# Performance work log

Hardware: AMD Instinct MI355X
Metric: run time of the kernel (lower is better)

The kernel has to match this reference:

```python
import jax, jax.numpy as jnp
import numpy as np

N, C, F, E = 32768, 256, 1024, 16
TOP_K = 2


def setup_inputs() -> dict:
    key = jax.random.key(0)
    k_x, k_gw, k_w1, k_w2 = jax.random.split(key, 4)
    x = jax.random.normal(k_x, (N, C), dtype=jnp.float32)
    gate_W = jax.random.normal(k_gw, (E, C), dtype=jnp.float32) * 0.01  # nn.init.normal_(std=0.01)
    gate_b = jnp.zeros((E,), dtype=jnp.float32)
    W1 = jax.random.normal(k_w1, (E, C, F), dtype=jnp.float32) * 0.02
    b1 = jnp.zeros((E, F), dtype=jnp.float32)
    W2 = jax.random.normal(k_w2, (E, F, C), dtype=jnp.float32) * 0.02
    b2 = jnp.zeros((E, C), dtype=jnp.float32)
    return {"x": x, "gate_W": gate_W, "gate_b": gate_b,
            "W1": W1, "b1": b1, "W2": W2, "b2": b2}


def reference(x, gate_W, gate_b, W1, b1, W2, b2):
    # Gating (eval mode: no gaussian noise)
    gate_logits = x @ gate_W.T + gate_b                       # [N, E]
    gate_probs = jax.nn.softmax(gate_logits, axis=-1)
    gate_entropy = -(gate_probs * jnp.log(gate_probs + 1e-8)).sum(axis=-1).mean()

    topk_val, topk_idx = jax.lax.top_k(gate_logits, TOP_K)   # [N, K]
    gate_weights = jax.nn.softmax(topk_val, axis=-1)          # softmax over the top-k logits

    # Dense all-expert FFN compute (matches the torch stack over experts)
    h = jax.nn.relu(jnp.einsum('nc,ecf->enf', x, W1) + b1[:, None, :])   # [E, N, F]
    expert_outputs = jnp.einsum('enf,efc->enc', h, W2) + b2[:, None, :]  # [E, N, C]

    # Gather top-k expert outputs per token and combine
    eo = jnp.transpose(expert_outputs, (1, 0, 2))             # [N, E, C]
    selected = jnp.take_along_axis(eo, topk_idx[:, :, None], axis=1)  # [N, K, C]
    out = (gate_weights[:, :, None] * selected).sum(axis=1)  # [N, C]

    # default args: return_gate=False, return_entropy=True
    return out, gate_entropy
```

## Files before the change

### kernel.cpp

```cpp
#include <hip/hip_runtime.h>
#include <hip/hip_bf16.h>
#include <math.h>

#define N_TOK 32768
#define C_DIM 256
#define F_DIM 1024
#define E_NUM 16
#define TILE_R 128
#define NCH 32
#define NBLK 544

typedef unsigned short u16;
typedef unsigned int u32;
typedef __attribute__((ext_vector_type(4))) u16 u16x4;
typedef __attribute__((ext_vector_type(8))) u16 u16x8;
typedef __attribute__((ext_vector_type(8))) short bf16x8;
typedef __attribute__((ext_vector_type(4))) u32 u32x4;
typedef __attribute__((ext_vector_type(16))) float f32x16;

#define AS1 __attribute__((address_space(1)))
#define AS3 __attribute__((address_space(3)))

__device__ __forceinline__ void gload16(const void* g, void* lds) {
    __builtin_amdgcn_global_load_lds((const AS1 u32*)(uintptr_t)g,
                                     (AS3 u32*)(u32)(uintptr_t)lds, 16, 0, 0);
}

__device__ __forceinline__ u16 f2bf(float f) {
    union { float f; u32 u; } v; v.f = f;
    u32 r = v.u + 0x7fffu + ((v.u >> 16) & 1u);
    return (u16)(r >> 16);
}

__device__ __forceinline__ float bf2f(u16 b) {
    union { u32 u; float f; } v; v.u = ((u32)b) << 16;
    return v.f;
}


__global__ __launch_bounds__(256) void gate_kernel(
    const float* __restrict__ x, const float* __restrict__ gW,
    const float* __restrict__ gb, float* __restrict__ ent_out,
    int* __restrict__ tidx, float* __restrict__ tw, int* __restrict__ counts,
    u16* __restrict__ xb)
{
    __shared__ float gws[E_NUM * C_DIM];
    __shared__ float gbs[E_NUM];
    __shared__ float went[4];
    __shared__ int lc[E_NUM];
    int tid = threadIdx.x;

    for (int i = tid; i < E_NUM * C_DIM / 4; i += 256)
        ((float4*)gws)[i] = ((const float4*)gW)[i];
    if (tid < E_NUM) { gbs[tid] = gb[tid]; lc[tid] = 0; }
    __syncthreads();

    int tok = tid >> 2, q = tid & 3;
    int n = blockIdx.x * 64 + tok;
    const float* xr = x + (size_t)n * C_DIM;

    float4 xv[16];
    #pragma unroll
    for (int j = 0; j < 16; j++)
        xv[j] = *(const float4*)(xr + j * 16 + q * 4);

    #pragma unroll
    for (int j = 0; j < 16; j++) {
        u16x4 o;
        o[0] = f2bf(xv[j].x); o[1] = f2bf(xv[j].y);
        o[2] = f2bf(xv[j].z); o[3] = f2bf(xv[j].w);
        *(u16x4*)(xb + (size_t)n * C_DIM + j * 16 + q * 4) = o;
    }

    float lg[E_NUM];
    #pragma unroll
    for (int e = 0; e < E_NUM; e++) lg[e] = 0.f;
    #pragma unroll
    for (int j = 0; j < 16; j++) {
        #pragma unroll
        for (int e = 0; e < E_NUM; e++) {
            float4 g = *(const float4*)(gws + e * C_DIM + j * 16 + q * 4);
            lg[e] += xv[j].x * g.x + xv[j].y * g.y + xv[j].z * g.z + xv[j].w * g.w;
        }
    }
    #pragma unroll
    for (int e = 0; e < E_NUM; e++) {
        lg[e] += __shfl_xor(lg[e], 1);
        lg[e] += __shfl_xor(lg[e], 2);
        lg[e] += gbs[e];
    }

    float m = lg[0];
    #pragma unroll
    for (int e = 1; e < E_NUM; e++) m = fmaxf(m, lg[e]);
    float s = 0.f, ex[E_NUM];
    #pragma unroll
    for (int e = 0; e < E_NUM; e++) { ex[e] = __expf(lg[e] - m); s += ex[e]; }
    float inv = 1.f / s;
    float ent = 0.f;
    #pragma unroll
    for (int e = 0; e < E_NUM; e++) {
        float p = ex[e] * inv;
        ent -= p * logf(p + 1e-8f);
    }

    float v0 = -1e30f, v1 = -1e30f;
    int i0 = 0, i1 = 0;
    #pragma unroll
    for (int e = 0; e < E_NUM; e++) {
        float l = lg[e];
        if (l > v0) { v1 = v0; i1 = i0; v0 = l; i0 = e; }
        else if (l > v1) { v1 = l; i1 = e; }
    }
    if (q == 0) {
        float w1e = __expf(v1 - v0);
        float z = 1.f + w1e;
        tidx[2 * n] = i0; tidx[2 * n + 1] = i1;
        tw[2 * n] = 1.f / z; tw[2 * n + 1] = w1e / z;
        atomicAdd(&lc[i0], 1);
        atomicAdd(&lc[i1], 1);
    }

    float v = ent;
    for (int off = 32; off > 0; off >>= 1) v += __shfl_down(v, off);
    int wid = tid >> 6, lane = tid & 63;
    if (lane == 0) went[wid] = v;
    __syncthreads();
    if (tid == 0)
        atomicAdd(ent_out, (went[0] + went[1] + went[2] + went[3]) * (1.0f / (4.0f * N_TOK)));
    if (tid < E_NUM && lc[tid]) atomicAdd(&counts[tid], lc[tid]);
}

__global__ void prefix_kernel(const int* __restrict__ counts,
                              int* __restrict__ offs, int* __restrict__ tp)
{
    if (threadIdx.x == 0 && blockIdx.x == 0) {
        int o = 0, t = 0;
        offs[0] = 0; tp[0] = 0;
        for (int e = 0; e < E_NUM; e++) {
            o += counts[e];
            t += (counts[e] + TILE_R - 1) / TILE_R;
            offs[e + 1] = o;
            tp[e + 1] = t;
        }
    }
}

__global__ __launch_bounds__(256) void scatter_kernel(
    const int* __restrict__ tidx, const float* __restrict__ tw,
    const int* __restrict__ offs, int* __restrict__ fill,
    int* __restrict__ tok, float* __restrict__ wgt, int* __restrict__ pairpos)
{
    __shared__ int lc[E_NUM], lbase[E_NUM];
    int tid = threadIdx.x;
    if (tid < E_NUM) lc[tid] = 0;
    __syncthreads();
    int n = blockIdx.x * 256 + tid;
    int e0 = tidx[2 * n], e1 = tidx[2 * n + 1];
    int r0 = atomicAdd(&lc[e0], 1);
    int r1 = atomicAdd(&lc[e1], 1);
    __syncthreads();
    if (tid < E_NUM) lbase[tid] = offs[tid] + atomicAdd(&fill[tid], lc[tid]);
    __syncthreads();
    int p0 = lbase[e0] + r0, p1 = lbase[e1] + r1;
    tok[p0] = n; wgt[p0] = tw[2 * n];     pairpos[2 * n] = p0;
    tok[p1] = n; wgt[p1] = tw[2 * n + 1]; pairpos[2 * n + 1] = p1;
}

__global__ __launch_bounds__(256) void tcvt_w1f(
    const float* __restrict__ W1, u16* __restrict__ w1f)
{
    __shared__ float t[256][33];
    int e = blockIdx.x, ft = blockIdx.y;
    int tid = threadIdx.x;
    const float* src = W1 + ((size_t)e * C_DIM) * F_DIM + (size_t)tid * F_DIM + ft * 32;
    #pragma unroll
    for (int j = 0; j < 8; j++) {
        float4 v = *(const float4*)(src + j * 4);
        t[tid][j * 4] = v.x; t[tid][j * 4 + 1] = v.y;
        t[tid][j * 4 + 2] = v.z; t[tid][j * 4 + 3] = v.w;
    }
    __syncthreads();
    int l = tid & 63, ksq = tid >> 6;
    #pragma unroll
    for (int p = 0; p < 4; p++) {
        int ks = ksq * 4 + p;
        int c0 = ks * 16 + (l >> 5) * 8;
        u16x8 o;
        #pragma unroll
        for (int j = 0; j < 8; j++) o[j] = f2bf(t[c0 + j][l & 31]);
        *(u16x8*)(w1f + ((size_t)((e * 32 + ft) * 16 + ks)) * 512 + l * 8) = o;
    }
}

__global__ __launch_bounds__(256) void tcvt_w2f(
    const float* __restrict__ W2, u16* __restrict__ w2f)
{
    __shared__ float t[256][33];
    int e = blockIdx.x, ct = blockIdx.y, fq = blockIdx.z;
    int tid = threadIdx.x;
    const float* src = W2 + ((size_t)e * F_DIM + fq * 256 + tid) * C_DIM + ct * 32;
    #pragma unroll
    for (int j = 0; j < 8; j++) {
        float4 v = *(const float4*)(src + j * 4);
        t[tid][j * 4] = v.x; t[tid][j * 4 + 1] = v.y;
        t[tid][j * 4 + 2] = v.z; t[tid][j * 4 + 3] = v.w;
    }
    __syncthreads();
    int l = tid & 63, kq = tid >> 6;
    #pragma unroll
    for (int p = 0; p < 4; p++) {
        int kfl = kq * 4 + p;
        int f0 = kfl * 16 + (l >> 5) * 8;
        u16x8 o;
        #pragma unroll
        for (int j = 0; j < 8; j++) o[j] = f2bf(t[f0 + j][l & 31]);
        *(u16x8*)(w2f + ((size_t)((e * 8 + ct) * 64 + fq * 16 + kfl)) * 512 + l * 8) = o;
    }
}

#define B1S_OFF 65536

#define STAGE_CHUNK(CHN, NBUF)                                                \
    {                                                                         \
        _Pragma("unroll")                                                     \
        for (int i = 0; i < 4; i++) {                                         \
            int ks = (wid << 2) + i;                                          \
            gload16(w1fe + (((size_t)((CHN) << 4) + ks) << 9) + (lane << 3),  \
                    (NBUF) + (ks << 10));                                     \
        }                                                                     \
        _Pragma("unroll")                                                     \
        for (int i = 0; i < 4; i++) {                                         \
            int g = (wid << 2) + i;                                           \
            int ct = g >> 1, s2 = g & 1;                                      \
            gload16(w2fe + (((size_t)(ct << 6) + ((CHN) << 1) + s2) << 9) + (lane << 3), \
                    (NBUF) + 16384 + (g << 10));                              \
        }                                                                     \
    }

template <int MODE>
__global__ __launch_bounds__(256, 2) void ffn_mfma(
    const u16* __restrict__ xb, const u16* __restrict__ w1f,
    const u16* __restrict__ w2f, const float* __restrict__ b1,
    const float* __restrict__ b2, const int* __restrict__ tok,
    const float* __restrict__ wgt, const int* __restrict__ offs,
    const int* __restrict__ tp, u16* __restrict__ ybuf,
    float* __restrict__ out)
{
    __shared__ __align__(1024) char smem[70656];
    int* s_tok = (int*)(smem + 69632);
    float* s_w = (float*)(smem + 70144);
    float* b1s = (float*)(smem + B1S_OFF);

    int bidx = blockIdx.x;
    int b = (bidx & 7) * (NBLK / 8) + (bidx >> 3);
    if (b >= tp[E_NUM]) return;
    int e = 0;
    while (b >= tp[e + 1]) e++;
    int base = offs[e] + ((b - tp[e]) << 7);
    int rows = offs[e + 1] - base; if (rows > TILE_R) rows = TILE_R;

    int tid = threadIdx.x;
    int lane = tid & 63, wid = tid >> 6;
    int hi = lane >> 5;

    const u16* w1fe = w1f + ((size_t)e << 9) * 512;
    const u16* w2fe = w2f + ((size_t)e << 9) * 512;
    const float* b1e = b1 + e * F_DIM;
    const float* b2e = b2 + e * C_DIM;

    if (tid < TILE_R) {
        int src = (tid < rows) ? base + tid : base;
        s_tok[tid] = tok[src];
        s_w[tid] = (tid < rows) ? wgt[src] : 0.f;
    }
    ((float4*)b1s)[tid] = ((const float4*)b1e)[tid];
    __syncthreads();

    #pragma unroll
    for (int i = 0; i < 16; i++) {
        int idx2 = (wid << 4) + i;
        int row = ((idx2 >> 4) << 5) + (lane & 31);
        gload16(xb + ((size_t)s_tok[row] << 8) + ((idx2 & 15) << 4) + (hi << 3),
                smem + (idx2 << 10));
    }
    asm volatile("s_waitcnt vmcnt(0)" ::: "memory");
    __syncthreads();

    bf16x8 xr[16];
    #pragma unroll
    for (int ks = 0; ks < 16; ks++)
        xr[ks] = *(const bf16x8*)(smem + (wid << 14) + (ks << 10) + (lane << 4));
    __syncthreads();

    STAGE_CHUNK(0, smem)
    asm volatile("s_waitcnt vmcnt(0)" ::: "memory");
    __syncthreads();

    f32x16 acc2[8];
    #pragma unroll
    for (int ct = 0; ct < 8; ct++) acc2[ct] = (f32x16)(0.0f);

    for (int ch = 0; ch < NCH; ch++) {
        int cur = ch & 1;
        const char* cbuf = smem + (cur << 15);

        if (ch + 1 < NCH) {
            char* nbuf = smem + ((cur ^ 1) << 15);
            STAGE_CHUNK(ch + 1, nbuf)
        }

        const char* w1b = cbuf + (lane << 4);
        f32x16 acc1a = (f32x16)(0.0f), acc1b = (f32x16)(0.0f);
        #pragma unroll
        for (int ks = 0; ks < 8; ks++) {
            bf16x8 a0 = *(const bf16x8*)(w1b + ((2 * ks) << 10));
            bf16x8 a1 = *(const bf16x8*)(w1b + ((2 * ks + 1) << 10));
            acc1a = __builtin_amdgcn_mfma_f32_32x32x16_bf16(a0, xr[2 * ks], acc1a, 0, 0, 0);
            acc1b = __builtin_amdgcn_mfma_f32_32x32x16_bf16(a1, xr[2 * ks + 1], acc1b, 0, 0, 0);
        }

        float h[16];
        #pragma unroll
        for (int r = 0; r < 16; r++) {
            int fl = (r & 3) + ((r >> 2) << 3) + (hi << 2);
            h[r] = fmaxf(acc1a[r] + acc1b[r] + b1s[(ch << 5) + fl], 0.f);
        }
        u32 w[8];
        #pragma unroll
        for (int t = 0; t < 8; t++)
            asm("v_cvt_pk_bf16_f32 %0, %1, %2" : "=v"(w[t]) : "v"(h[2 * t]), "v"(h[2 * t + 1]));
        asm volatile("v_permlane32_swap_b32 %0, %1" : "+v"(w[0]), "+v"(w[2]));
        asm volatile("v_permlane32_swap_b32 %0, %1" : "+v"(w[1]), "+v"(w[3]));
        asm volatile("v_permlane32_swap_b32 %0, %1" : "+v"(w[4]), "+v"(w[6]));
        asm volatile("v_permlane32_swap_b32 %0, %1" : "+v"(w[5]), "+v"(w[7]));
        union { u32x4 u; bf16x8 v; } fr0, fr1;
        fr0.u = (u32x4){w[0], w[1], w[2], w[3]};
        fr1.u = (u32x4){w[4], w[5], w[6], w[7]};

        const char* w2b = cbuf + 16384 + (lane << 4);
        #pragma unroll
        for (int ctl = 0; ctl < 8; ctl++) {
            bf16x8 a0 = *(const bf16x8*)(w2b + ((ctl << 1) << 10));
            bf16x8 a1 = *(const bf16x8*)(w2b + (((ctl << 1) + 1) << 10));
            acc2[ctl] = __builtin_amdgcn_mfma_f32_32x32x16_bf16(a0, fr0.v, acc2[ctl], 0, 0, 0);
            acc2[ctl] = __builtin_amdgcn_mfma_f32_32x32x16_bf16(a1, fr1.v, acc2[ctl], 0, 0, 0);
        }

        asm volatile("s_waitcnt vmcnt(0) lgkmcnt(0)" ::: "memory");
        __builtin_amdgcn_s_barrier();
        __builtin_amdgcn_sched_barrier(0);
    }

    int m = (wid << 5) + (lane & 31);
    if (m < rows) {
        if (MODE == 0) {
            u16* yr = ybuf + ((size_t)(base + m) << 8);
            #pragma unroll
            for (int ctl = 0; ctl < 8; ctl++) {
                #pragma unroll
                for (int rq = 0; rq < 4; rq++) {
                    int c = (ctl << 5) + (rq << 3) + (hi << 2);
                    u16x4 o;
                    o[0] = f2bf(acc2[ctl][4 * rq]);
                    o[1] = f2bf(acc2[ctl][4 * rq + 1]);
                    o[2] = f2bf(acc2[ctl][4 * rq + 2]);
                    o[3] = f2bf(acc2[ctl][4 * rq + 3]);
                    *(u16x4*)(yr + c) = o;
                }
            }
        } else {
            float wgt_m = s_w[m];
            float* orow = out + ((size_t)s_tok[m] << 8);
            #pragma unroll
            for (int ctl = 0; ctl < 8; ctl++) {
                #pragma unroll
                for (int rq = 0; rq < 4; rq++) {
                    int c = (ctl << 5) + (rq << 3) + (hi << 2);
                    #pragma unroll
                    for (int l2 = 0; l2 < 4; l2++)
                        atomicAdd(&orow[c + l2],
                                  wgt_m * (acc2[ctl][4 * rq + l2] + b2e[c + l2]));
                }
            }
        }
    }
}

__global__ __launch_bounds__(256) void combine_kernel(
    const u16* __restrict__ ybuf, const int* __restrict__ tidx,
    const float* __restrict__ tw, const int* __restrict__ pairpos,
    const float* __restrict__ b2, float* __restrict__ out)
{
    int idx = blockIdx.x * 256 + threadIdx.x;
    int n = idx >> 6;
    int q = (idx & 63) << 2;
    int e0 = tidx[2 * n], e1 = tidx[2 * n + 1];
    float w0 = tw[2 * n], w1 = tw[2 * n + 1];
    int p0 = pairpos[2 * n], p1 = pairpos[2 * n + 1];
    u16x4 y0 = *(const u16x4*)(ybuf + ((size_t)p0 << 8) + q);
    u16x4 y1 = *(const u16x4*)(ybuf + ((size_t)p1 << 8) + q);
    float4 c0 = *(const float4*)(b2 + (e0 << 8) + q);
    float4 c1 = *(const float4*)(b2 + (e1 << 8) + q);
    float4 o;
    o.x = w0 * (bf2f(y0[0]) + c0.x) + w1 * (bf2f(y1[0]) + c1.x);
    o.y = w0 * (bf2f(y0[1]) + c0.y) + w1 * (bf2f(y1[1]) + c1.y);
    o.z = w0 * (bf2f(y0[2]) + c0.z) + w1 * (bf2f(y1[2]) + c1.z);
    o.w = w0 * (bf2f(y0[3]) + c0.w) + w1 * (bf2f(y1[3]) + c1.w);
    *(float4*)(out + ((size_t)n << 8) + q) = o;
}

extern "C" void kernel_launch(void* const* d_in, const int* in_sizes, int n_in,
                              void* d_out, int out_size, void* d_ws, size_t ws_size,
                              hipStream_t stream)
{
    const float* x   = (const float*)d_in[0];
    const float* gW  = (const float*)d_in[1];
    const float* gb  = (const float*)d_in[2];
    const float* W1  = (const float*)d_in[3];
    const float* b1  = (const float*)d_in[4];
    const float* W2  = (const float*)d_in[5];
    const float* b2  = (const float*)d_in[6];
    float* out = (float*)d_out;

    char* ws = (char*)d_ws;
    int*   topk_idx = (int*)(ws + 0);
    float* topk_w   = (float*)(ws + 262144);
    int*   tok      = (int*)(ws + 524288);
    float* wgt      = (float*)(ws + 786432);
    int*   pairpos  = (int*)(ws + 1048576);
    int*   counts   = (int*)(ws + 1310720);
    int*   fill     = (int*)(ws + 1310784);
    int*   offs     = (int*)(ws + 1310848);
    int*   tp       = (int*)(ws + 1310916);

    const size_t XB_OFF  = 2097152;
    const size_t W1F_OFF = 18874368;
    const size_t W2F_OFF = 27262976;
    const size_t Y_OFF   = 35651584;
    const size_t WS_FULL = Y_OFF + (size_t)2 * N_TOK * C_DIM * 2;

    u16* xb  = (u16*)(ws + XB_OFF);
    u16* w1f = (u16*)(ws + W1F_OFF);
    u16* w2f = (u16*)(ws + W2F_OFF);
    u16* ybuf = (u16*)(ws + Y_OFF);

    int mode = (ws_size >= WS_FULL) ? 0 : 1;

    float* ent_out = out + (size_t)N_TOK * C_DIM;

    if (mode == 0) {
        hipMemsetAsync(ent_out, 0, sizeof(float), stream);
    } else {
        hipMemsetAsync(d_out, 0, (size_t)(N_TOK * C_DIM + 1) * sizeof(float), stream);
    }
    hipMemsetAsync(counts, 0, 2 * E_NUM * sizeof(int), stream);

    gate_kernel<<<N_TOK / 64, 256, 0, stream>>>(x, gW, gb, ent_out,
                                                topk_idx, topk_w, counts, xb);
    prefix_kernel<<<1, 64, 0, stream>>>(counts, offs, tp);
    scatter_kernel<<<N_TOK / 256, 256, 0, stream>>>(topk_idx, topk_w, offs,
                                                    fill, tok, wgt, pairpos);
    tcvt_w1f<<<dim3(E_NUM, 32), 256, 0, stream>>>(W1, w1f);
    tcvt_w2f<<<dim3(E_NUM, 8, 4), 256, 0, stream>>>(W2, w2f);

    if (mode == 0) {
        ffn_mfma<0><<<NBLK, 256, 0, stream>>>(xb, w1f, w2f, b1, b2, tok, wgt,
                                              offs, tp, ybuf, out);
        combine_kernel<<<N_TOK * 64 / 256, 256, 0, stream>>>(ybuf, topk_idx,
                                                             topk_w, pairpos, b2, out);
    } else {
        ffn_mfma<1><<<NBLK, 256, 0, stream>>>(xb, w1f, w2f, b1, b2, tok, wgt,
                                              offs, tp, ybuf, out);
    }
}
```

Baseline: 181.7 us.

## Double rows per block so each wave computes two 32-row tiles sharing weight loads

Raises the token tile from 128 to 256 rows per block. Each wave now holds two sets of x fragments and accumulators, so every W1/W2 chunk staged into LDS feeds twice as many MFMAs. This halves weight traffic per token and the number of blocks. In exchange, register pressure roughly doubles, forcing one block per CU instead of two. There are also fewer, larger blocks, which risks tail imbalance and more padding waste on each expert's last tile.

```diff
diff --git a/kernel.cpp b/kernel.cpp
--- a/kernel.cpp
+++ b/kernel.cpp
@@ -6,9 +6,9 @@
 #define C_DIM 256
 #define F_DIM 1024
 #define E_NUM 16
-#define TILE_R 128
+#define TILE_R 256
 #define NCH 32
-#define NBLK 544
+#define NBLK 272
 
 typedef unsigned short u16;
 typedef unsigned int u32;
@@ -238,8 +238,62 @@
         }                                                                     \
     }
 
+#define REPACK(AA, AB, FR0, FR1)                                              \
+    {                                                                         \
+        float h[16];                                                          \
+        _Pragma("unroll")                                                     \
+        for (int r = 0; r < 16; r++) {                                        \
+            int fl = (r & 3) + ((r >> 2) << 3) + (hi << 2);                   \
+            h[r] = fmaxf((AA)[r] + (AB)[r] + b1s[(ch << 5) + fl], 0.f);       \
+        }                                                                     \
+        u32 w[8];                                                             \
+        _Pragma("unroll")                                                     \
+        for (int t = 0; t < 8; t++)                                           \
+            asm("v_cvt_pk_bf16_f32 %0, %1, %2" : "=v"(w[t]) : "v"(h[2 * t]), "v"(h[2 * t + 1])); \
+        asm volatile("v_permlane32_swap_b32 %0, %1" : "+v"(w[0]), "+v"(w[2]));\
+        asm volatile("v_permlane32_swap_b32 %0, %1" : "+v"(w[1]), "+v"(w[3]));\
+        asm volatile("v_permlane32_swap_b32 %0, %1" : "+v"(w[4]), "+v"(w[6]));\
+        asm volatile("v_permlane32_swap_b32 %0, %1" : "+v"(w[5]), "+v"(w[7]));\
+        (FR0).u = (u32x4){w[0], w[1], w[2], w[3]};                            \
+        (FR1).u = (u32x4){w[4], w[5], w[6], w[7]};                            \
+    }
+
+#define EPILOGUE_TILE(ACC, MIDX)                                              \
+    if ((MIDX) < rows) {                                                      \
+        if (MODE == 0) {                                                      \
+            u16* yr = ybuf + ((size_t)(base + (MIDX)) << 8);                  \
+            _Pragma("unroll")                                                 \
+            for (int ctl = 0; ctl < 8; ctl++) {                               \
+                _Pragma("unroll")                                             \
+                for (int rq = 0; rq < 4; rq++) {                              \
+                    int c = (ctl << 5) + (rq << 3) + (hi << 2);               \
+                    u16x4 o;                                                  \
+                    o[0] = f2bf((ACC)[ctl][4 * rq]);                          \
+                    o[1] = f2bf((ACC)[ctl][4 * rq + 1]);                      \
+                    o[2] = f2bf((ACC)[ctl][4 * rq + 2]);                      \
+                    o[3] = f2bf((ACC)[ctl][4 * rq + 3]);                      \
+                    *(u16x4*)(yr + c) = o;                                    \
+                }                                                             \
+            }                                                                 \
+        } else {                                                              \
+            float wgt_m = s_w[(MIDX)];                                        \
+            float* orow = out + ((size_t)s_tok[(MIDX)] << 8);                 \
+            _Pragma("unroll")                                                 \
+            for (int ctl = 0; ctl < 8; ctl++) {                               \
+                _Pragma("unroll")                                             \
+                for (int rq = 0; rq < 4; rq++) {                              \
+                    int c = (ctl << 5) + (rq << 3) + (hi << 2);               \
+                    _Pragma("unroll")                                         \
+                    for (int l2 = 0; l2 < 4; l2++)                            \
+                        atomicAdd(&orow[c + l2],                              \
+                                  wgt_m * ((ACC)[ctl][4 * rq + l2] + b2e[c + l2])); \
+                }                                                             \
+            }                                                                 \
+        }                                                                     \
+    }
+
 template <int MODE>
-__global__ __launch_bounds__(256, 2) void ffn_mfma(
+__global__ __launch_bounds__(256, 1) void ffn_mfma(
     const u16* __restrict__ xb, const u16* __restrict__ w1f,
     const u16* __restrict__ w2f, const float* __restrict__ b1,
     const float* __restrict__ b2, const int* __restrict__ tok,
@@ -247,9 +301,9 @@
     const int* __restrict__ tp, u16* __restrict__ ybuf,
     float* __restrict__ out)
 {
-    __shared__ __align__(1024) char smem[70656];
+    __shared__ __align__(1024) char smem[71680];
     int* s_tok = (int*)(smem + 69632);
-    float* s_w = (float*)(smem + 70144);
+    float* s_w = (float*)(smem + 70656);
     float* b1s = (float*)(smem + B1S_OFF);
 
     int bidx = blockIdx.x;
@@ -257,7 +311,7 @@
     if (b >= tp[E_NUM]) return;
     int e = 0;
     while (b >= tp[e + 1]) e++;
-    int base = offs[e] + ((b - tp[e]) << 7);
+    int base = offs[e] + ((b - tp[e]) << 8);
     int rows = offs[e + 1] - base; if (rows > TILE_R) rows = TILE_R;
 
     int tid = threadIdx.x;
@@ -277,29 +331,40 @@
     ((float4*)b1s)[tid] = ((const float4*)b1e)[tid];
     __syncthreads();
 
-    #pragma unroll
-    for (int i = 0; i < 16; i++) {
-        int idx2 = (wid << 4) + i;
-        int row = ((idx2 >> 4) << 5) + (lane & 31);
-        gload16(xb + ((size_t)s_tok[row] << 8) + ((idx2 & 15) << 4) + (hi << 3),
-                smem + (idx2 << 10));
-    }
-    asm volatile("s_waitcnt vmcnt(0)" ::: "memory");
-    __syncthreads();
-
-    bf16x8 xr[16];
-    #pragma unroll
-    for (int ks = 0; ks < 16; ks++)
-        xr[ks] = *(const bf16x8*)(smem + (wid << 14) + (ks << 10) + (lane << 4));
-    __syncthreads();
+    bf16x8 xrA[16], xrB[16];
+    #pragma unroll
+    for (int half = 0; half < 2; half++) {
+        #pragma unroll
+        for (int i = 0; i < 16; i++) {
+            int idx2 = (wid << 4) + i;
+            int row = ((idx2 >> 4) << 5) + (lane & 31) + (half << 7);
+            gload16(xb + ((size_t)s_tok[row] << 8) + ((idx2 & 15) << 4) + (hi << 3),
+                    smem + (idx2 << 10));
+        }
+        asm volatile("s_waitcnt vmcnt(0)" ::: "memory");
+        __syncthreads();
+        if (half == 0) {
+            #pragma unroll
+            for (int ks = 0; ks < 16; ks++)
+                xrA[ks] = *(const bf16x8*)(smem + (wid << 14) + (ks << 10) + (lane << 4));
+        } else {
+            #pragma unroll
+            for (int ks = 0; ks < 16; ks++)
+                xrB[ks] = *(const bf16x8*)(smem + (wid << 14) + (ks << 10) + (lane << 4));
+        }
+        __syncthreads();
+    }
 
     STAGE_CHUNK(0, smem)
     asm volatile("s_waitcnt vmcnt(0)" ::: "memory");
     __syncthreads();
 
-    f32x16 acc2[8];
-    #pragma unroll
-    for (int ct = 0; ct < 8; ct++) acc2[ct] = (f32x16)(0.0f);
+    f32x16 acc2A[8], acc2B[8];
+    #pragma unroll
+    for (int ct = 0; ct < 8; ct++) {
+        acc2A[ct] = (f32x16)(0.0f);
+        acc2B[ct] = (f32x16)(0.0f);
+    }
 
     for (int ch = 0; ch < NCH; ch++) {
         int cur = ch & 1;
@@ -311,40 +376,31 @@
         }
 
         const char* w1b = cbuf + (lane << 4);
-        f32x16 acc1a = (f32x16)(0.0f), acc1b = (f32x16)(0.0f);
+        f32x16 aAa = (f32x16)(0.0f), aAb = (f32x16)(0.0f);
+        f32x16 aBa = (f32x16)(0.0f), aBb = (f32x16)(0.0f);
         #pragma unroll
         for (int ks = 0; ks < 8; ks++) {
             bf16x8 a0 = *(const bf16x8*)(w1b + ((2 * ks) << 10));
             bf16x8 a1 = *(const bf16x8*)(w1b + ((2 * ks + 1) << 10));
-            acc1a = __builtin_amdgcn_mfma_f32_32x32x16_bf16(a0, xr[2 * ks], acc1a, 0, 0, 0);
-            acc1b = __builtin_amdgcn_mfma_f32_32x32x16_bf16(a1, xr[2 * ks + 1], acc1b, 0, 0, 0);
-        }
-
-        float h[16];
-        #pragma unroll
-        for (int r = 0; r < 16; r++) {
-            int fl = (r & 3) + ((r >> 2) << 3) + (hi << 2);
-            h[r] = fmaxf(acc1a[r] + acc1b[r] + b1s[(ch << 5) + fl], 0.f);
-        }
-        u32 w[8];
-        #pragma unroll
-        for (int t = 0; t < 8; t++)
-            asm("v_cvt_pk_bf16_f32 %0, %1, %2" : "=v"(w[t]) : "v"(h[2 * t]), "v"(h[2 * t + 1]));
-        asm volatile("v_permlane32_swap_b32 %0, %1" : "+v"(w[0]), "+v"(w[2]));
-        asm volatile("v_permlane32_swap_b32 %0, %1" : "+v"(w[1]), "+v"(w[3]));
-        asm volatile("v_permlane32_swap_b32 %0, %1" : "+v"(w[4]), "+v"(w[6]));
-        asm volatile("v_permlane32_swap_b32 %0, %1" : "+v"(w[5]), "+v"(w[7]));
-        union { u32x4 u; bf16x8 v; } fr0, fr1;
-        fr0.u = (u32x4){w[0], w[1], w[2], w[3]};
-        fr1.u = (u32x4){w[4], w[5], w[6], w[7]};
+            aAa = __builtin_amdgcn_mfma_f32_32x32x16_bf16(a0, xrA[2 * ks], aAa, 0, 0, 0);
+            aBa = __builtin_amdgcn_mfma_f32_32x32x16_bf16(a0, xrB[2 * ks], aBa, 0, 0, 0);
+            aAb = __builtin_amdgcn_mfma_f32_32x32x16_bf16(a1, xrA[2 * ks + 1], aAb, 0, 0, 0);
+            aBb = __builtin_amdgcn_mfma_f32_32x32x16_bf16(a1, xrB[2 * ks + 1], aBb, 0, 0, 0);
+        }
+
+        union { u32x4 u; bf16x8 v; } frA0, frA1, frB0, frB1;
+        REPACK(aAa, aAb, frA0, frA1)
+        REPACK(aBa, aBb, frB0, frB1)
 
         const char* w2b = cbuf + 16384 + (lane << 4);
         #pragma unroll
         for (int ctl = 0; ctl < 8; ctl++) {
             bf16x8 a0 = *(const bf16x8*)(w2b + ((ctl << 1) << 10));
             bf16x8 a1 = *(const bf16x8*)(w2b + (((ctl << 1) + 1) << 10));
-            acc2[ctl] = __builtin_amdgcn_mfma_f32_32x32x16_bf16(a0, fr0.v, acc2[ctl], 0, 0, 0);
-            acc2[ctl] = __builtin_amdgcn_mfma_f32_32x32x16_bf16(a1, fr1.v, acc2[ctl], 0, 0, 0);
+            acc2A[ctl] = __builtin_amdgcn_mfma_f32_32x32x16_bf16(a0, frA0.v, acc2A[ctl], 0, 0, 0);
+            acc2A[ctl] = __builtin_amdgcn_mfma_f32_32x32x16_bf16(a1, frA1.v, acc2A[ctl], 0, 0, 0);
+            acc2B[ctl] = __builtin_amdgcn_mfma_f32_32x32x16_bf16(a0, frB0.v, acc2B[ctl], 0, 0, 0);
+            acc2B[ctl] = __builtin_amdgcn_mfma_f32_32x32x16_bf16(a1, frB1.v, acc2B[ctl], 0, 0, 0);
         }
 
         asm volatile("s_waitcnt vmcnt(0) lgkmcnt(0)" ::: "memory");
@@ -352,39 +408,10 @@
         __builtin_amdgcn_sched_barrier(0);
     }
 
-    int m = (wid << 5) + (lane & 31);
-    if (m < rows) {
-        if (MODE == 0) {
-            u16* yr = ybuf + ((size_t)(base + m) << 8);
-            #pragma unroll
-            for (int ctl = 0; ctl < 8; ctl++) {
-                #pragma unroll
-                for (int rq = 0; rq < 4; rq++) {
-                    int c = (ctl << 5) + (rq << 3) + (hi << 2);
-                    u16x4 o;
-                    o[0] = f2bf(acc2[ctl][4 * rq]);
-                    o[1] = f2bf(acc2[ctl][4 * rq + 1]);
-                    o[2] = f2bf(acc2[ctl][4 * rq + 2]);
-                    o[3] = f2bf(acc2[ctl][4 * rq + 3]);
-                    *(u16x4*)(yr + c) = o;
-                }
-            }
-        } else {
-            float wgt_m = s_w[m];
-            float* orow = out + ((size_t)s_tok[m] << 8);
-            #pragma unroll
-            for (int ctl = 0; ctl < 8; ctl++) {
-                #pragma unroll
-                for (int rq = 0; rq < 4; rq++) {
-                    int c = (ctl << 5) + (rq << 3) + (hi << 2);
-                    #pragma unroll
-                    for (int l2 = 0; l2 < 4; l2++)
-                        atomicAdd(&orow[c + l2],
-                                  wgt_m * (acc2[ctl][4 * rq + l2] + b2e[c + l2]));
-                }
-            }
-        }
-    }
+    int mA = (wid << 5) + (lane & 31);
+    int mB = mA + 128;
+    EPILOGUE_TILE(acc2A, mA)
+    EPILOGUE_TILE(acc2B, mB)
 }
 
 __global__ __launch_bounds__(256) void combine_kernel(
```

Result: slower. 329.2 us (+81.2%).

## Load expert weight fragments directly from global memory into registers, drop LDS staging

Applied to the files above, without the earlier changes.

Removes the double-buffered LDS staging of W1/W2 chunks and the per-chunk barrier. Each wave now reads its weight fragments straight from global memory (through the cache) into registers just before the MFMAs. This saves LDS traffic and workgroup synchronisation. In exchange, every wave re-reads the same weights, the loads are no longer prefetched a chunk ahead, and register pressure rises from the 16-entry fragment arrays.

```diff
diff --git a/kernel.cpp b/kernel.cpp
--- a/kernel.cpp
+++ b/kernel.cpp
@@ -221,23 +221,6 @@
 
 #define B1S_OFF 65536
 
-#define STAGE_CHUNK(CHN, NBUF)                                                \
-    {                                                                         \
-        _Pragma("unroll")                                                     \
-        for (int i = 0; i < 4; i++) {                                         \
-            int ks = (wid << 2) + i;                                          \
-            gload16(w1fe + (((size_t)((CHN) << 4) + ks) << 9) + (lane << 3),  \
-                    (NBUF) + (ks << 10));                                     \
-        }                                                                     \
-        _Pragma("unroll")                                                     \
-        for (int i = 0; i < 4; i++) {                                         \
-            int g = (wid << 2) + i;                                           \
-            int ct = g >> 1, s2 = g & 1;                                      \
-            gload16(w2fe + (((size_t)(ct << 6) + ((CHN) << 1) + s2) << 9) + (lane << 3), \
-                    (NBUF) + 16384 + (g << 10));                              \
-        }                                                                     \
-    }
-
 template <int MODE>
 __global__ __launch_bounds__(256, 2) void ffn_mfma(
     const u16* __restrict__ xb, const u16* __restrict__ w1f,
@@ -291,33 +274,25 @@
     #pragma unroll
     for (int ks = 0; ks < 16; ks++)
         xr[ks] = *(const bf16x8*)(smem + (wid << 14) + (ks << 10) + (lane << 4));
-    __syncthreads();
-
-    STAGE_CHUNK(0, smem)
-    asm volatile("s_waitcnt vmcnt(0)" ::: "memory");
-    __syncthreads();
 
     f32x16 acc2[8];
     #pragma unroll
     for (int ct = 0; ct < 8; ct++) acc2[ct] = (f32x16)(0.0f);
 
+    const u16* w1p = w1fe + (lane << 3);
+    const u16* w2p = w2fe + (lane << 3);
+
     for (int ch = 0; ch < NCH; ch++) {
-        int cur = ch & 1;
-        const char* cbuf = smem + (cur << 15);
-
-        if (ch + 1 < NCH) {
-            char* nbuf = smem + ((cur ^ 1) << 15);
-            STAGE_CHUNK(ch + 1, nbuf)
-        }
-
-        const char* w1b = cbuf + (lane << 4);
+        bf16x8 wf[16];
+        #pragma unroll
+        for (int k = 0; k < 16; k++)
+            wf[k] = *(const bf16x8*)(w1p + (((size_t)(ch << 4) + k) << 9));
+
         f32x16 acc1a = (f32x16)(0.0f), acc1b = (f32x16)(0.0f);
         #pragma unroll
         for (int ks = 0; ks < 8; ks++) {
-            bf16x8 a0 = *(const bf16x8*)(w1b + ((2 * ks) << 10));
-            bf16x8 a1 = *(const bf16x8*)(w1b + ((2 * ks + 1) << 10));
-            acc1a = __builtin_amdgcn_mfma_f32_32x32x16_bf16(a0, xr[2 * ks], acc1a, 0, 0, 0);
-            acc1b = __builtin_amdgcn_mfma_f32_32x32x16_bf16(a1, xr[2 * ks + 1], acc1b, 0, 0, 0);
+            acc1a = __builtin_amdgcn_mfma_f32_32x32x16_bf16(wf[2 * ks], xr[2 * ks], acc1a, 0, 0, 0);
+            acc1b = __builtin_amdgcn_mfma_f32_32x32x16_bf16(wf[2 * ks + 1], xr[2 * ks + 1], acc1b, 0, 0, 0);
         }
 
         float h[16];
@@ -338,18 +313,17 @@
         fr0.u = (u32x4){w[0], w[1], w[2], w[3]};
         fr1.u = (u32x4){w[4], w[5], w[6], w[7]};
 
-        const char* w2b = cbuf + 16384 + (lane << 4);
+        bf16x8 wg[16];
+        #pragma unroll
+        for (int g = 0; g < 16; g++) {
+            int ct = g >> 1, s2 = g & 1;
+            wg[g] = *(const bf16x8*)(w2p + (((size_t)(ct << 6) + (ch << 1) + s2) << 9));
+        }
         #pragma unroll
         for (int ctl = 0; ctl < 8; ctl++) {
-            bf16x8 a0 = *(const bf16x8*)(w2b + ((ctl << 1) << 10));
-            bf16x8 a1 = *(const bf16x8*)(w2b + (((ctl << 1) + 1) << 10));
-            acc2[ctl] = __builtin_amdgcn_mfma_f32_32x32x16_bf16(a0, fr0.v, acc2[ctl], 0, 0, 0);
-            acc2[ctl] = __builtin_amdgcn_mfma_f32_32x32x16_bf16(a1, fr1.v, acc2[ctl], 0, 0, 0);
-        }
-
-        asm volatile("s_waitcnt vmcnt(0) lgkmcnt(0)" ::: "memory");
-        __builtin_amdgcn_s_barrier();
-        __builtin_amdgcn_sched_barrier(0);
+            acc2[ctl] = __builtin_amdgcn_mfma_f32_32x32x16_bf16(wg[2 * ctl], fr0.v, acc2[ctl], 0, 0, 0);
+            acc2[ctl] = __builtin_amdgcn_mfma_f32_32x32x16_bf16(wg[2 * ctl + 1], fr1.v, acc2[ctl], 0, 0, 0);
+        }
     }
 
     int m = (wid << 5) + (lane & 31);
```

Result: slower. 257.2 us (+41.6%).

## Halve FFN tile to 64 rows with 2-wave blocks and single-buffered weights

Applied to the files above, without the earlier changes.

Cuts the FFN tile from 128 to 64 tokens per block, uses 128-thread blocks, and raises the grid from 544 to 1040 blocks so more blocks can be resident. It drops the double-buffered weight staging for a single buffer loaded at the top of each chunk, with wave 0 loading W1 and wave 1 loading W2. This shrinks LDS to allow more blocks per CU. In exchange, each weight chunk is reused across half as many tokens, which doubles weight traffic, and load latency is no longer overlapped with MFMA work inside a block. Other parts of the kernel not shown, such as the x staging loop indexed by wid and the MODE 1 output path, may still assume the old 4-wave layout.

```diff
diff --git a/kernel.cpp b/kernel.cpp
--- a/kernel.cpp
+++ b/kernel.cpp
@@ -6,9 +6,9 @@
 #define C_DIM 256
 #define F_DIM 1024
 #define E_NUM 16
-#define TILE_R 128
+#define TILE_R 64
 #define NCH 32
-#define NBLK 544
+#define NBLK 1040
 
 typedef unsigned short u16;
 typedef unsigned int u32;
@@ -219,27 +219,25 @@
     }
 }
 
-#define B1S_OFF 65536
-
-#define STAGE_CHUNK(CHN, NBUF)                                                \
-    {                                                                         \
+#define B1S_OFF 32768
+
+#define STAGE_CHUNK(CHN)                                                      \
+    if (wid == 0) {                                                           \
         _Pragma("unroll")                                                     \
-        for (int i = 0; i < 4; i++) {                                         \
-            int ks = (wid << 2) + i;                                          \
-            gload16(w1fe + (((size_t)((CHN) << 4) + ks) << 9) + (lane << 3),  \
-                    (NBUF) + (ks << 10));                                     \
-        }                                                                     \
+        for (int k = 0; k < 16; k++)                                          \
+            gload16(w1fe + (((size_t)((CHN) << 4) + k) << 9) + (lane << 3),   \
+                    smem + (k << 10));                                        \
+    } else {                                                                  \
         _Pragma("unroll")                                                     \
-        for (int i = 0; i < 4; i++) {                                         \
-            int g = (wid << 2) + i;                                           \
+        for (int g = 0; g < 16; g++) {                                        \
             int ct = g >> 1, s2 = g & 1;                                      \
             gload16(w2fe + (((size_t)(ct << 6) + ((CHN) << 1) + s2) << 9) + (lane << 3), \
-                    (NBUF) + 16384 + (g << 10));                              \
+                    smem + 16384 + (g << 10));                                \
         }                                                                     \
     }
 
 template <int MODE>
-__global__ __launch_bounds__(256, 2) void ffn_mfma(
+__global__ __launch_bounds__(128, 4) void ffn_mfma(
     const u16* __restrict__ xb, const u16* __restrict__ w1f,
     const u16* __restrict__ w2f, const float* __restrict__ b1,
     const float* __restrict__ b2, const int* __restrict__ tok,
@@ -247,9 +245,9 @@
     const int* __restrict__ tp, u16* __restrict__ ybuf,
     float* __restrict__ out)
 {
-    __shared__ __align__(1024) char smem[70656];
-    int* s_tok = (int*)(smem + 69632);
-    float* s_w = (float*)(smem + 70144);
+    __shared__ __align__(1024) char smem[38400];
+    int* s_tok = (int*)(smem + 36864);
+    float* s_w = (float*)(smem + 37120);
     float* b1s = (float*)(smem + B1S_OFF);
 
     int bidx = blockIdx.x;
@@ -257,7 +255,7 @@
     if (b >= tp[E_NUM]) return;
     int e = 0;
     while (b >= tp[e + 1]) e++;
-    int base = offs[e] + ((b - tp[e]) << 7);
+    int base = offs[e] + ((b - tp[e]) << 6);
     int rows = offs[e + 1] - base; if (rows > TILE_R) rows = TILE_R;
 
     int tid = threadIdx.x;
@@ -274,7 +272,9 @@
         s_tok[tid] = tok[src];
         s_w[tid] = (tid < rows) ? wgt[src] : 0.f;
     }
-    ((float4*)b1s)[tid] = ((const float4*)b1e)[tid];
+    #pragma unroll
+    for (int i = 0; i < 2; i++)
+        ((float4*)b1s)[tid + i * 128] = ((const float4*)b1e)[tid + i * 128];
     __syncthreads();
 
     #pragma unroll
@@ -293,24 +293,17 @@
         xr[ks] = *(const bf16x8*)(smem + (wid << 14) + (ks << 10) + (lane << 4));
     __syncthreads();
 
-    STAGE_CHUNK(0, smem)
-    asm volatile("s_waitcnt vmcnt(0)" ::: "memory");
-    __syncthreads();
-
     f32x16 acc2[8];
     #pragma unroll
     for (int ct = 0; ct < 8; ct++) acc2[ct] = (f32x16)(0.0f);
 
     for (int ch = 0; ch < NCH; ch++) {
-        int cur = ch & 1;
-        const char* cbuf = smem + (cur << 15);
-
-        if (ch + 1 < NCH) {
-            char* nbuf = smem + ((cur ^ 1) << 15);
-            STAGE_CHUNK(ch + 1, nbuf)
-        }
-
-        const char* w1b = cbuf + (lane << 4);
+        STAGE_CHUNK(ch)
+        asm volatile("s_waitcnt vmcnt(0)" ::: "memory");
+        __builtin_amdgcn_s_barrier();
+        __builtin_amdgcn_sched_barrier(0);
+
+        const char* w1b = smem + (lane << 4);
         f32x16 acc1a = (f32x16)(0.0f), acc1b = (f32x16)(0.0f);
         #pragma unroll
         for (int ks = 0; ks < 8; ks++) {
@@ -338,16 +331,16 @@
         fr0.u = (u32x4){w[0], w[1], w[2], w[3]};
         fr1.u = (u32x4){w[4], w[5], w[6], w[7]};
 
-        const char* w2b = cbuf + 16384 + (lane << 4);
+        const char* w2b = smem + 16384 + (lane << 4);
         #pragma unroll
         for (int ctl = 0; ctl < 8; ctl++) {
-            bf16x8 a0 = *(const bf16x8*)(w2b + ((ctl << 1) << 10));
-            bf16x8 a1 = *(const bf16x8*)(w2b + (((ctl << 1) + 1) << 10));
-            acc2[ctl] = __builtin_amdgcn_mfma_f32_32x32x16_bf16(a0, fr0.v, acc2[ctl], 0, 0, 0);
-            acc2[ctl] = __builtin_amdgcn_mfma_f32_32x32x16_bf16(a1, fr1.v, acc2[ctl], 0, 0, 0);
-        }
-
-        asm volatile("s_waitcnt vmcnt(0) lgkmcnt(0)" ::: "memory");
+            bf16x8 b0 = *(const bf16x8*)(w2b + ((ctl << 1) << 10));
+            bf16x8 b1v = *(const bf16x8*)(w2b + (((ctl << 1) + 1) << 10));
+            acc2[ctl] = __builtin_amdgcn_mfma_f32_32x32x16_bf16(b0, fr0.v, acc2[ctl], 0, 0, 0);
+            acc2[ctl] = __builtin_amdgcn_mfma_f32_32x32x16_bf16(b1v, fr1.v, acc2[ctl], 0, 0, 0);
+        }
+
+        asm volatile("s_waitcnt lgkmcnt(0)" ::: "memory");
         __builtin_amdgcn_s_barrier();
         __builtin_amdgcn_sched_barrier(0);
     }
@@ -465,12 +458,12 @@
     tcvt_w2f<<<dim3(E_NUM, 8, 4), 256, 0, stream>>>(W2, w2f);
 
     if (mode == 0) {
-        ffn_mfma<0><<<NBLK, 256, 0, stream>>>(xb, w1f, w2f, b1, b2, tok, wgt,
+        ffn_mfma<0><<<NBLK, 128, 0, stream>>>(xb, w1f, w2f, b1, b2, tok, wgt,
                                               offs, tp, ybuf, out);
         combine_kernel<<<N_TOK * 64 / 256, 256, 0, stream>>>(ybuf, topk_idx,
                                                              topk_w, pairpos, b2, out);
     } else {
-        ffn_mfma<1><<<NBLK, 256, 0, stream>>>(xb, w1f, w2f, b1, b2, tok, wgt,
+        ffn_mfma<1><<<NBLK, 128, 0, stream>>>(xb, w1f, w2f, b1, b2, tok, wgt,
                                               offs, tp, ybuf, out);
     }
 }
```

Measured after the change: 233.1 us. +28.3%, slower.
